# Kernel tuning notes

Measured on AMD Instinct MI355X. Metric: run time of the kernel, lower is better.

Reference implementation:

```python
import jax, jax.numpy as jnp
import numpy as np

NEG = -1000000.0


def setup_inputs() -> dict:
    key = jax.random.key(0)
    k0, k1, k2, k3, k4 = jax.random.split(key, 5)
    b, c, h, w = 4, 256, 64, 64
    dvt_c = 768
    x = jax.random.normal(k0, (b, c, h, w), jnp.float32)
    dvtfeats = jax.random.normal(k1, (b, dvt_c, h, w), jnp.float32)
    coarse = (jax.random.uniform(k2, (b, 1, h, w)) > 0.5).astype(jnp.float32)
    mask = jnp.repeat(jnp.repeat(coarse, 8, axis=2), 8, axis=3)  # [b,1,512,512]
    # K_conv: Conv2d(c+768 -> c, 1x1) with bias; fuse: Conv2d(2c -> c, 1x1) no bias
    K_w = jax.random.normal(k3, (c, c + dvt_c), jnp.float32) * 0.02
    K_b = jnp.zeros((c,), jnp.float32)
    fuse_w = jax.random.normal(k4, (c, 2 * c), jnp.float32) * 0.02
    return {"x": x, "mask": mask, "dvtfeats": dvtfeats, "K_w": K_w, "K_b": K_b, "fuse_w": fuse_w}


def _conv1x1(inp, w, b=None):
    out = jnp.einsum('bihw,oi->bohw', inp, w)
    if b is not None:
        out = out + b[None, :, None, None]
    return out


def _forward(x, mask, dvtfeats, K_w, K_b, fuse_w):
    b, c, h, w = x.shape
    n = h * w
    # maxpool(8,8) then binarize
    m = mask.reshape(b, 1, h, 8, w, 8).max(axis=(3, 5))
    m = (m > 0).astype(x.dtype)            # [b,1,h,w] foreground mask
    bm = 1.0 - m                            # background mask
    # K_conv applied once (original applies the same conv twice to the same input)
    feats = _conv1x1(jnp.concatenate([x, dvtfeats], axis=1), K_w, K_b)  # [b,c,h,w]
    K = (feats * bm).reshape(b, c, n)
    Q = (feats * m).reshape(b, c, n).transpose(0, 2, 1)  # [b,n,c]
    K = K / (jnp.linalg.norm(K, axis=1, keepdims=True) + 1e-8)
    Q = Q / (jnp.linalg.norm(Q, axis=2, keepdims=True) + 1e-8)
    V = (x * bm).reshape(b, c, n)
    score = jnp.einsum('bqc,bck->bqk', Q, K) * 20.0       # [b,n,n] cosine sims
    qm = m.reshape(b, 1, n)    # query mask (foreground)
    km = bm.reshape(b, 1, n)   # key mask (background)
    score = score + (1.0 - km) * NEG + (1.0 - qm).transpose(0, 2, 1) * NEG
    att = jax.nn.softmax(score, axis=-1)
    att = att * qm.transpose(0, 2, 1) * km                # zero out invalid rows/cols
    # att_fore[b,c,q] = sum_k V[b,c,k] * att[b,q,k]
    att_fore = jnp.einsum('bck,bqk->bcq', V, att).reshape(b, c, h, w)
    fused = _conv1x1(jnp.concatenate([att_fore, x], axis=1), fuse_w)
    visatt = att.sum(axis=1).reshape(b, 1, h, w)          # sum over query dim
    attmask = jnp.repeat(jnp.repeat(visatt, 8, axis=2), 8, axis=3)  # nearest upsample x8
    attmask = attmask / attmask.max()
    out = fused * m + x * (1.0 - m)
    return out, attmask


def reference(x, mask, dvtfeats, K_w, K_b, fuse_w):
    return _forward(x, mask, dvtfeats, K_w, K_b, fuse_w)
```

## Files before the change

### kernel.cpp

```cpp
#include <hip/hip_runtime.h>
#include <hip/hip_bf16.h>

typedef __attribute__((ext_vector_type(8))) short short8;
typedef __attribute__((ext_vector_type(4))) float f32x4;
typedef unsigned int uint;
typedef unsigned short ushort;

constexpr int BATCH = 4;
constexpr int CH    = 256;
constexpr int N     = 4096;
constexpr int DVC   = 768;
constexpr int CIN   = 1024;
constexpr int KC    = 512;
constexpr int PBS   = 5 * 1024 * 1024;
constexpr int QCH   = 32;
constexpr int SPLITK = 4;

constexpr size_t OFF_M    = 0;
constexpr size_t OFF_INV  = 64ull << 10;
constexpr size_t OFF_VIS  = 128ull << 10;
constexpr size_t OFF_MAXV = 192ull << 10;
constexpr size_t OFF_CNT  = 196ull << 10;
constexpr size_t OFF_FGI  = 256ull << 10;
constexpr size_t OFF_BGI  = 320ull << 10;
constexpr size_t OFF_P2S  = 384ull << 10;
constexpr size_t OFF_KMC  = 448ull << 10;
constexpr size_t OFF_PART = 1ull << 20;
constexpr size_t OFF_KWB  = 5ull << 20;
constexpr size_t OFF_FWB  = OFF_KWB + (512ull << 10);
constexpr size_t OFF_XT   = 6ull << 20;
constexpr size_t OFF_QC   = 38ull << 20;
constexpr size_t OFF_KCC  = 46ull << 20;
constexpr size_t OFF_XC   = 54ull << 20;
constexpr size_t OFF_AFT  = 62ull << 20;
constexpr size_t OFF_P    = 70ull << 20;
constexpr size_t OFF_AFP  = 110ull << 20;

__device__ __forceinline__ ushort f2bf(float f) {
    __hip_bfloat16 h = __float2bfloat16(f);
    return __builtin_bit_cast(ushort, h);
}
__device__ __forceinline__ float bf2f(ushort u) {
    uint v = (uint)u << 16;
    return __builtin_bit_cast(float, v);
}

typedef const __attribute__((address_space(1))) uint* gptr_t;
typedef __attribute__((address_space(3))) uint* lptr_t;
__device__ __forceinline__ void gload_lds16(const void* g, void* l) {
    __builtin_amdgcn_global_load_lds((gptr_t)g, (lptr_t)l, 16, 0, 0);
}

template<int WM, int WN>
__device__ __forceinline__ void gemm_core(
    const ushort* __restrict__ A0, int lda, int m0,
    const ushort* __restrict__ B0, int ldb0, int kend0,
    const ushort* __restrict__ B1, int ldb1,
    int n0, int K,
    ushort* AsL, ushort* BsL, f32x4 acc[4][4])
{
    constexpr int NW = WM * WN, BM = WM * 64, BN = WN * 64;
    const int t = threadIdx.x, lane = t & 63, wid = t >> 6;
    const int wm = (wid / WN) * 64, wn = (wid % WN) * 64;

    for (int k0 = 0; k0 < K; k0 += 64) {
        #pragma unroll
        for (int c = wid; c < BM / 8; c += NW) {
            const ushort* g = A0 + (size_t)(m0 + c * 8 + (lane >> 3)) * lda + (k0 + (lane & 7) * 8);
            gload_lds16(g, AsL + c * 512);
        }
        const ushort* Bsrc = (k0 < kend0) ? B0 : B1;
        const int ldb = (k0 < kend0) ? ldb0 : ldb1;
        const int kc  = (k0 < kend0) ? k0 : (k0 - kend0);
        #pragma unroll
        for (int c = wid; c < BN / 8; c += NW) {
            const ushort* g = Bsrc + (size_t)(n0 + c * 8 + (lane >> 3)) * ldb + (kc + (lane & 7) * 8);
            gload_lds16(g, BsL + c * 512);
        }
        __syncthreads();

        const int ra = wm + (lane & 15), rb = wn + (lane & 15), ko = (lane >> 4) * 8;
        #pragma unroll
        for (int kk = 0; kk < 64; kk += 32) {
            short8 a[4], b[4];
            #pragma unroll
            for (int i = 0; i < 4; i++) a[i] = *(const short8*)(AsL + (ra + i * 16) * 64 + kk + ko);
            #pragma unroll
            for (int j = 0; j < 4; j++) b[j] = *(const short8*)(BsL + (rb + j * 16) * 64 + kk + ko);
            #pragma unroll
            for (int i = 0; i < 4; i++)
                #pragma unroll
                for (int j = 0; j < 4; j++)
                    acc[i][j] = __builtin_amdgcn_mfma_f32_16x16x32_bf16(a[i], b[j], acc[i][j], 0, 0, 0);
        }
        __syncthreads();
    }
}

__device__ __forceinline__ void zero_acc(f32x4 acc[4][4]) {
    f32x4 z = {0.f, 0.f, 0.f, 0.f};
    #pragma unroll
    for (int i = 0; i < 4; i++)
        #pragma unroll
        for (int j = 0; j < 4; j++) acc[i][j] = z;
}

__global__ void k_maskpool(const float* __restrict__ mask, float* __restrict__ m,
                           float* __restrict__ vis, uint* __restrict__ maxv)
{
    int idx = blockIdx.x * 256 + threadIdx.x;
    int b = idx >> 12, p = idx & 4095;
    int y = p >> 6, x = p & 63;
    const float* base = mask + (size_t)b * 512 * 512 + (y * 8) * 512 + x * 8;
    float mx = 0.f;
    for (int dy = 0; dy < 8; dy++) {
        #pragma unroll
        for (int dx = 0; dx < 8; dx++) mx = fmaxf(mx, base[dy * 512 + dx]);
    }
    m[idx] = (mx > 0.f) ? 1.f : 0.f;
    vis[idx] = 0.f;
    if (idx == 0) maxv[0] = 0u;
}

__global__ __launch_bounds__(256) void k_scan(
    const float* __restrict__ m, int* __restrict__ fgi, int* __restrict__ bgi,
    int* __restrict__ counts, float* __restrict__ kmc, int* __restrict__ p2s)
{
    const int b = blockIdx.x, t = threadIdx.x;
    const float* mb = m + (size_t)b * N;
    __shared__ int sfg[256], sbg[256];
    bool isf[16];
    int cf = 0, cb_ = 0;
    #pragma unroll
    for (int j = 0; j < 16; j++) {
        bool f = mb[t * 16 + j] != 0.f;
        isf[j] = f; cf += f ? 1 : 0; cb_ += f ? 0 : 1;
    }
    sfg[t] = cf; sbg[t] = cb_;
    __syncthreads();
    for (int off = 1; off < 256; off <<= 1) {
        int vf = (t >= off) ? sfg[t - off] : 0;
        int vb = (t >= off) ? sbg[t - off] : 0;
        __syncthreads();
        sfg[t] += vf; sbg[t] += vb;
        __syncthreads();
    }
    int basef = sfg[t] - cf, baseb = sbg[t] - cb_;
    int nfg = sfg[255], nbg = sbg[255];
    #pragma unroll
    for (int j = 0; j < 16; j++) {
        int p = t * 16 + j;
        if (isf[j]) { fgi[b * N + basef] = p; p2s[b * N + p] = basef | (1 << 30); basef++; }
        else        { bgi[b * N + baseb] = p; p2s[b * N + p] = baseb; baseb++; }
    }
    if (t == 0) {
        counts[b * 4 + 0] = nfg;
        counts[b * 4 + 1] = (nfg + 127) & ~127;
        counts[b * 4 + 2] = nbg;
        counts[b * 4 + 3] = (nbg + 127) & ~127;
    }
    for (int j = t; j < N; j += 256) kmc[b * N + j] = (j < nbg) ? 1.f : 0.f;
}

__global__ void k_wconv(const float* __restrict__ Kw, const float* __restrict__ fw,
                        ushort* __restrict__ Kwb, ushort* __restrict__ fwb)
{
    int i = blockIdx.x * 256 + threadIdx.x;
    if (i < CH * CIN) Kwb[i] = f2bf(Kw[i]);
    else              fwb[i - CH * CIN] = f2bf(fw[i - CH * CIN]);
}

__global__ __launch_bounds__(256) void k_tr(const float* __restrict__ src,
                                            ushort* __restrict__ dst, int C)
{
    __shared__ float Ls[64][65];
    const int ci0 = blockIdx.x * 64, n0 = blockIdx.y * 64, b = blockIdx.z;
    const float* s = src + (size_t)b * C * 4096;
    const int t = threadIdx.x;
    #pragma unroll
    for (int it = 0; it < 4; it++) {
        int f4 = it * 256 + t;
        int r = f4 >> 4, c4 = f4 & 15;
        float4 v = *(const float4*)(s + (size_t)(ci0 + r) * 4096 + n0 + c4 * 4);
        Ls[r][c4 * 4 + 0] = v.x; Ls[r][c4 * 4 + 1] = v.y;
        Ls[r][c4 * 4 + 2] = v.z; Ls[r][c4 * 4 + 3] = v.w;
    }
    __syncthreads();
    ushort* d = dst + (size_t)b * 4096 * C;
    #pragma unroll
    for (int it = 0; it < 8; it++) {
        int p = it * 256 + t;
        int rn = p >> 5, cc2 = p & 31;
        uint val = (uint)f2bf(Ls[cc2 * 2][rn]) | ((uint)f2bf(Ls[cc2 * 2 + 1][rn]) << 16);
        *(uint*)(d + (size_t)(n0 + rn) * C + ci0 + cc2 * 2) = val;
    }
}

__global__ __launch_bounds__(256) void k_vgather(
    const ushort* __restrict__ xT, const int* __restrict__ bgi,
    const int* __restrict__ counts, ushort* __restrict__ xc)
{
    __shared__ ushort Xs[64][264];
    const int b = blockIdx.y;
    const int ki0 = blockIdx.x * 64;
    const int nbg = counts[b * 4 + 2], nbgp = counts[b * 4 + 3];
    if (ki0 >= nbgp) return;
    const int t = threadIdx.x;
    const int j = t >> 2, part = t & 3;
    const int ki = ki0 + j;
    if (ki < nbg) {
        const ushort* src = xT + ((size_t)b * N + bgi[(size_t)b * N + ki]) * CH + part * 64;
        #pragma unroll
        for (int q = 0; q < 8; q++)
            *(uint4*)&Xs[j][part * 64 + q * 8] = *(const uint4*)(src + q * 8);
    } else {
        uint4 z = {0, 0, 0, 0};
        #pragma unroll
        for (int q = 0; q < 8; q++)
            *(uint4*)&Xs[j][part * 64 + q * 8] = z;
    }
    __syncthreads();
    const int c = t;
    ushort* dst = xc + ((size_t)b * CH + c) * N + ki0;
    uint w[32];
    #pragma unroll
    for (int jj = 0; jj < 32; jj++)
        w[jj] = (uint)Xs[2 * jj][c] | ((uint)Xs[2 * jj + 1][c] << 16);
    #pragma unroll
    for (int q = 0; q < 8; q++) {
        uint4 o = { w[q * 4], w[q * 4 + 1], w[q * 4 + 2], w[q * 4 + 3] };
        *(uint4*)(dst + q * 8) = o;
    }
}

__global__ __launch_bounds__(256) void k_feats(
    const ushort* __restrict__ Kwb, const ushort* __restrict__ xT,
    const float* __restrict__ dvt, const float* __restrict__ Kb,
    const int* __restrict__ p2s, ushort* __restrict__ Qc, ushort* __restrict__ Kc)
{
    __shared__ ushort As[256 * 64];
    __shared__ ushort Bs[64 * 64];
    __shared__ float  Ls[64][65];
    __shared__ float  red[4][64];
    const int b = blockIdx.z;
    const int n0 = blockIdx.x * 64;
    const int t = threadIdx.x, lane = t & 63, wid = t >> 6;
    const ushort* xTb = xT + (size_t)b * N * CH;
    const float* dvb = dvt + (size_t)b * DVC * N;
    f32x4 acc[4][4]; zero_acc(acc);

    for (int k0 = 0; k0 < 256; k0 += 64) {
        #pragma unroll
        for (int c = wid; c < 32; c += 4)
            gload_lds16(Kwb + (size_t)(c * 8 + (lane >> 3)) * CIN + k0 + (lane & 7) * 8, As + c * 512);
        #pragma unroll
        for (int c = wid; c < 8; c += 4)
            gload_lds16(xTb + (size_t)(n0 + c * 8 + (lane >> 3)) * CH + k0 + (lane & 7) * 8, Bs + c * 512);
        __syncthreads();
        const int ra = wid * 64 + (lane & 15), rb = lane & 15, ko = (lane >> 4) * 8;
        #pragma unroll
        for (int kk = 0; kk < 64; kk += 32) {
            short8 a[4], bb[4];
            #pragma unroll
            for (int i = 0; i < 4; i++) a[i] = *(const short8*)(As + (ra + i * 16) * 64 + kk + ko);
            #pragma unroll
            for (int j = 0; j < 4; j++) bb[j] = *(const short8*)(Bs + (rb + j * 16) * 64 + kk + ko);
            #pragma unroll
            for (int i = 0; i < 4; i++)
                #pragma unroll
                for (int j = 0; j < 4; j++)
                    acc[i][j] = __builtin_amdgcn_mfma_f32_16x16x32_bf16(a[i], bb[j], acc[i][j], 0, 0, 0);
        }
        __syncthreads();
    }
    for (int k0 = 256; k0 < 1024; k0 += 64) {
        #pragma unroll
        for (int c = wid; c < 32; c += 4)
            gload_lds16(Kwb + (size_t)(c * 8 + (lane >> 3)) * CIN + k0 + (lane & 7) * 8, As + c * 512);
        const float* dsrc = dvb + (size_t)(k0 - 256) * N + n0;
        #pragma unroll
        for (int it = 0; it < 4; it++) {
            int f4 = it * 256 + t;
            int r = f4 >> 4, c4 = (f4 & 15) * 4;
            float4 v = *(const float4*)(dsrc + (size_t)r * N + c4);
            Ls[r][c4 + 0] = v.x; Ls[r][c4 + 1] = v.y;
            Ls[r][c4 + 2] = v.z; Ls[r][c4 + 3] = v.w;
        }
        __syncthreads();
        {
            int rn = t >> 2;
            int ks = (t & 3) * 16;
            #pragma unroll
            for (int j2 = 0; j2 < 8; j2++) {
                int kk = ks + j2 * 2;
                uint val = (uint)f2bf(Ls[kk][rn]) | ((uint)f2bf(Ls[kk + 1][rn]) << 16);
                int idx = (rn * 64 + kk) ^ ((rn & 7) << 3);
                *(uint*)(Bs + idx) = val;
            }
        }
        __syncthreads();
        const int ra = wid * 64 + (lane & 15), rb = lane & 15, ko = (lane >> 4) * 8;
        #pragma unroll
        for (int kk = 0; kk < 64; kk += 32) {
            short8 a[4], bb[4];
            #pragma unroll
            for (int i = 0; i < 4; i++) a[i] = *(const short8*)(As + (ra + i * 16) * 64 + kk + ko);
            #pragma unroll
            for (int j = 0; j < 4; j++) {
                int row = rb + j * 16;
                int idx = (row * 64 + kk + ko) ^ ((row & 7) << 3);
                bb[j] = *(const short8*)(Bs + idx);
            }
            #pragma unroll
            for (int i = 0; i < 4; i++)
                #pragma unroll
                for (int j = 0; j < 4; j++)
                    acc[i][j] = __builtin_amdgcn_mfma_f32_16x16x32_bf16(a[i], bb[j], acc[i][j], 0, 0, 0);
        }
        __syncthreads();
    }

    const int wm = wid * 64;
    float sj[4] = {0.f, 0.f, 0.f, 0.f};
    #pragma unroll
    for (int i = 0; i < 4; i++) {
        int mbase = wm + i * 16 + ((lane >> 4) * 4);
        float4 bias = *(const float4*)(Kb + mbase);
        #pragma unroll
        for (int j = 0; j < 4; j++) {
            acc[i][j][0] += bias.x; acc[i][j][1] += bias.y;
            acc[i][j][2] += bias.z; acc[i][j][3] += bias.w;
            sj[j] += acc[i][j][0] * acc[i][j][0] + acc[i][j][1] * acc[i][j][1]
                   + acc[i][j][2] * acc[i][j][2] + acc[i][j][3] * acc[i][j][3];
        }
    }
    #pragma unroll
    for (int j = 0; j < 4; j++) {
        sj[j] += __shfl_xor(sj[j], 16);
        sj[j] += __shfl_xor(sj[j], 32);
    }
    if (lane < 16) {
        #pragma unroll
        for (int j = 0; j < 4; j++) red[wid][j * 16 + lane] = sj[j];
    }
    __syncthreads();
    const int* pb = p2s + (size_t)b * N + n0;
    #pragma unroll
    for (int j = 0; j < 4; j++) {
        int n = j * 16 + (lane & 15);
        float s = red[0][n] + red[1][n] + red[2][n] + red[3][n];
        float invn = 1.f / (sqrtf(s) + 1e-8f);
        int sl = pb[n];
        ushort* dst = (sl & (1 << 30)) ? Qc : Kc;
        int slot = sl & 0x3FFFFFFF;
        ushort* drow = dst + ((size_t)b * N + slot) * CH;
        #pragma unroll
        for (int i = 0; i < 4; i++) {
            int mbase = wm + i * 16 + ((lane >> 4) * 4);
            ushort4 o = { f2bf(acc[i][j][0] * invn), f2bf(acc[i][j][1] * invn),
                          f2bf(acc[i][j][2] * invn), f2bf(acc[i][j][3] * invn) };
            *(ushort4*)(drow + mbase) = o;
        }
    }
}

__global__ __launch_bounds__(128) void k_score(
    const ushort* __restrict__ Qc, const ushort* __restrict__ Kc,
    const float* __restrict__ kmc, const int* __restrict__ counts,
    ushort* __restrict__ P)
{
    const int b = blockIdx.z;
    const int nfgp = counts[b * 4 + 1], nbgp = counts[b * 4 + 3];
    const int m0 = blockIdx.y * 128;
    const int n0 = blockIdx.x * 64;
    if (m0 >= nfgp || n0 >= nbgp) return;
    __shared__ ushort SH[(128 + 64) * 64];
    const int t = threadIdx.x, lane = t & 63, wid = t >> 6;
    const ushort* Qb = Qc + (size_t)b * N * CH;
    const ushort* Kb_ = Kc + (size_t)b * N * CH;
    f32x4 acc[4][4]; zero_acc(acc);
    gemm_core<2, 1>(Qb, CH, m0, Kb_, CH, CH, Kb_, CH, n0, CH, SH, SH + 128 * 64, acc);

    const int wm = wid * 64;
    float km[4];
    #pragma unroll
    for (int j = 0; j < 4; j++) km[j] = kmc[(size_t)b * N + n0 + j * 16 + (lane & 15)];

    ushort* Cs = SH;
    #pragma unroll
    for (int i = 0; i < 4; i++) {
        int rbase = wm + i * 16 + ((lane >> 4) * 4);
        #pragma unroll
        for (int j = 0; j < 4; j++) {
            int cl = j * 16 + (lane & 15);
            #pragma unroll
            for (int r = 0; r < 4; r++) {
                float p = (km[j] != 0.f) ? __expf(20.f * acc[i][j][r] - 20.f) : 0.f;
                Cs[(rbase + r) * 64 + cl] = f2bf(p);
            }
        }
    }
    __syncthreads();
    ushort* Pb = P + (size_t)b * PBS;
    #pragma unroll
    for (int it = 0; it < 8; it++) {
        int v8 = it * 128 + t;
        int row = v8 >> 3, c8 = (v8 & 7) * 8;
        *(uint4*)(Pb + (size_t)(m0 + row) * nbgp + n0 + c8) = *(const uint4*)(Cs + row * 64 + c8);
    }
}

__global__ __launch_bounds__(256) void k_rowsum(
    const ushort* __restrict__ P, const int* __restrict__ counts,
    float* __restrict__ inv)
{
    const int t = threadIdx.x, lane = t & 63, wid = t >> 6;
    const int g = blockIdx.x * 4 + wid;
    const int b = g >> 12, qi = g & 4095;
    const int nfgp = counts[b * 4 + 1], nbgp = counts[b * 4 + 3];
    if (qi >= nfgp) return;
    const ushort* row = P + (size_t)b * PBS + (size_t)qi * nbgp;
    float s = 0.f;
    for (int it = 0; it < 8; it++) {
        int base = it * 512 + lane * 8;
        if (base < nbgp) {
            uint4 v = *(const uint4*)(row + base);
            const ushort* u = (const ushort*)&v;
            #pragma unroll
            for (int e = 0; e < 8; e++) s += bf2f(u[e]);
        }
    }
    #pragma unroll
    for (int mm = 1; mm < 64; mm <<= 1) s += __shfl_xor(s, mm);
    if (lane == 0) inv[g] = (s > 0.f) ? 1.f / s : 0.f;
}

__global__ __launch_bounds__(256) void k_att_fore(
    const ushort* __restrict__ xc, const ushort* __restrict__ P,
    const int* __restrict__ counts, ushort* __restrict__ AFp)
{
    const int b = blockIdx.z & (BATCH - 1);
    const int sk = blockIdx.z / BATCH;
    const int nfgp = counts[b * 4 + 1], nbgp = counts[b * 4 + 3];
    const int n0 = blockIdx.x * 64;
    if (n0 >= nfgp) return;
    const int kchunk = ((nbgp / 64 + SPLITK - 1) / SPLITK) * 64;
    const int k0s = sk * kchunk;
    const int len = min(kchunk, nbgp - k0s);

    const int lane = threadIdx.x & 63, wid = threadIdx.x >> 6;
    f32x4 acc[4][4]; zero_acc(acc);
    if (len > 0) {
        __shared__ ushort SH[(256 + 64) * 64];
        const ushort* Pb = P + (size_t)b * PBS + k0s;
        gemm_core<4, 1>(xc + (size_t)b * CH * N + k0s, N, 0,
                        Pb, nbgp, 1 << 30, Pb, nbgp,
                        n0, len, SH, SH + 256 * 64, acc);
    }
    ushort* Ap = AFp + ((size_t)(sk * BATCH + b) * N) * CH;
    const int wm = wid * 64;
    #pragma unroll
    for (int j = 0; j < 4; j++) {
        int qi = n0 + j * 16 + (lane & 15);
        #pragma unroll
        for (int i = 0; i < 4; i++) {
            int mbase = wm + i * 16 + ((lane >> 4) * 4);
            ushort4 o = { f2bf(acc[i][j][0]), f2bf(acc[i][j][1]),
                          f2bf(acc[i][j][2]), f2bf(acc[i][j][3]) };
            *(ushort4*)(Ap + (size_t)qi * CH + mbase) = o;
        }
    }
}

__global__ __launch_bounds__(256) void k_afreduce(
    const ushort* __restrict__ AFp, const float* __restrict__ inv,
    const int* __restrict__ fgi, const int* __restrict__ counts,
    ushort* __restrict__ AFt)
{
    const int t = threadIdx.x, lane = t & 63, wid = t >> 6;
    const int g = blockIdx.x * 4 + wid;
    const int b = g >> 12, qi = g & 4095;
    if (qi >= counts[b * 4]) return;
    const size_t rowoff = ((size_t)b * N + qi) * CH + lane * 4;
    float s0 = 0.f, s1 = 0.f, s2 = 0.f, s3 = 0.f;
    #pragma unroll
    for (int sk = 0; sk < SPLITK; sk++) {
        ushort4 v = *(const ushort4*)(AFp + (size_t)sk * BATCH * N * CH + rowoff);
        s0 += bf2f(v.x); s1 += bf2f(v.y); s2 += bf2f(v.z); s3 += bf2f(v.w);
    }
    float iq = inv[g];
    int q = fgi[g];
    ushort4 o = { f2bf(s0 * iq), f2bf(s1 * iq), f2bf(s2 * iq), f2bf(s3 * iq) };
    *(ushort4*)(AFt + ((size_t)b * N + q) * CH + lane * 4) = o;
}

__global__ __launch_bounds__(128) void k_fused(
    const ushort* __restrict__ fwb, const ushort* __restrict__ AFt,
    const ushort* __restrict__ xT, const float* __restrict__ x,
    const float* __restrict__ m_, float* __restrict__ out)
{
    __shared__ ushort SH[(64 + 128) * 64];
    const int b = blockIdx.z;
    const int n0 = blockIdx.x * 128, m0 = blockIdx.y * 64;
    const int lane = threadIdx.x & 63, wid = threadIdx.x >> 6;
    const int wn = (wid & 1) * 64;
    f32x4 acc[4][4]; zero_acc(acc);
    gemm_core<1, 2>(fwb, KC, m0,
                    AFt + (size_t)b * N * CH, CH, CH,
                    xT + (size_t)b * N * CH, CH,
                    n0, KC, SH, SH + 64 * 64, acc);
    const float* mb = m_ + (size_t)b * N;
    const float* xc_ = x + (size_t)b * CH * N;
    float* ob = out + (size_t)b * CH * N;
    #pragma unroll
    for (int j = 0; j < 4; j++) {
        int n = n0 + wn + j * 16 + (lane & 15);
        float mv = mb[n];
        #pragma unroll
        for (int i = 0; i < 4; i++) {
            int mbase = m0 + i * 16 + ((lane >> 4) * 4);
            #pragma unroll
            for (int r = 0; r < 4; r++) {
                int c = mbase + r;
                ob[(size_t)c * N + n] = (mv != 0.f) ? acc[i][j][r] : xc_[(size_t)c * N + n];
            }
        }
    }
}

__global__ __launch_bounds__(256) void k_colsum(
    const ushort* __restrict__ P, const float* __restrict__ inv,
    const int* __restrict__ counts, float* __restrict__ part)
{
    const int b = blockIdx.z, qc = blockIdx.y, t = threadIdx.x;
    const int nfg = counts[b * 4], nbgp = counts[b * 4 + 3];
    const int ki0 = blockIdx.x * 2048 + t * 8;
    if (ki0 >= nbgp) return;
    const int qchunk = (nfg + QCH - 1) / QCH;
    const int q0 = qc * qchunk, q1 = min(q0 + qchunk, nfg);
    const ushort* base = P + (size_t)b * PBS + (size_t)q0 * nbgp + ki0;
    const float* ib = inv + (size_t)b * N;
    float acc[8] = {};
    int q = q0;
    for (; q + 4 <= q1; q += 4) {
        uint4 v0 = *(const uint4*)(base);
        uint4 v1 = *(const uint4*)(base + (size_t)nbgp);
        uint4 v2 = *(const uint4*)(base + 2 * (size_t)nbgp);
        uint4 v3 = *(const uint4*)(base + 3 * (size_t)nbgp);
        float i0 = ib[q], i1 = ib[q + 1], i2 = ib[q + 2], i3 = ib[q + 3];
        const ushort* u0 = (const ushort*)&v0;
        const ushort* u1 = (const ushort*)&v1;
        const ushort* u2 = (const ushort*)&v2;
        const ushort* u3 = (const ushort*)&v3;
        #pragma unroll
        for (int e = 0; e < 8; e++)
            acc[e] += bf2f(u0[e]) * i0 + bf2f(u1[e]) * i1 + bf2f(u2[e]) * i2 + bf2f(u3[e]) * i3;
        base += 4 * (size_t)nbgp;
    }
    for (; q < q1; q++) {
        uint4 v = *(const uint4*)(base);
        float iq = ib[q];
        const ushort* u = (const ushort*)&v;
        #pragma unroll
        for (int e = 0; e < 8; e++) acc[e] += bf2f(u[e]) * iq;
        base += (size_t)nbgp;
    }
    float* pp = part + (size_t)qc * (BATCH * N) + (size_t)b * N + ki0;
    float4 o0 = {acc[0], acc[1], acc[2], acc[3]};
    float4 o1 = {acc[4], acc[5], acc[6], acc[7]};
    *(float4*)(pp)     = o0;
    *(float4*)(pp + 4) = o1;
}

__global__ void k_colsum_final(const float* __restrict__ part, const int* __restrict__ bgi,
                               const int* __restrict__ counts, float* __restrict__ vis,
                               uint* __restrict__ maxv)
{
    int g = blockIdx.x * 256 + threadIdx.x;
    int b = g >> 12, ki = g & 4095;
    int t = threadIdx.x;
    float s = 0.f;
    if (ki < counts[b * 4 + 2]) {
        #pragma unroll
        for (int j = 0; j < QCH; j++) s += part[(size_t)j * (BATCH * N) + g];
        vis[(size_t)b * N + bgi[(size_t)b * N + ki]] = s;
    }
    __shared__ float red[256];
    red[t] = s; __syncthreads();
    for (int st = 128; st > 0; st >>= 1) { if (t < st) red[t] = fmaxf(red[t], red[t + st]); __syncthreads(); }
    if (t == 0) atomicMax(maxv, __float_as_uint(red[0]));
}

__global__ void k_attmask(const float* __restrict__ vis, const float* __restrict__ maxv,
                          float* __restrict__ amask)
{
    int idx = blockIdx.x * 256 + threadIdx.x;
    int b = idx >> 18;
    int r = idx & 262143;
    int Y = r >> 9, X = r & 511;
    amask[idx] = vis[(size_t)b * N + (Y >> 3) * 64 + (X >> 3)] / maxv[0];
}

extern "C" void kernel_launch(void* const* d_in, const int* in_sizes, int n_in,
                              void* d_out, int out_size, void* d_ws, size_t ws_size,
                              hipStream_t stream)
{
    const float* x    = (const float*)d_in[0];
    const float* mask = (const float*)d_in[1];
    const float* dvt  = (const float*)d_in[2];
    const float* Kw   = (const float*)d_in[3];
    const float* Kb   = (const float*)d_in[4];
    const float* fw   = (const float*)d_in[5];
    float* out = (float*)d_out;

    char* ws = (char*)d_ws;
    float*  m    = (float*)(ws + OFF_M);
    float*  inv  = (float*)(ws + OFF_INV);
    float*  vis  = (float*)(ws + OFF_VIS);
    float*  maxv = (float*)(ws + OFF_MAXV);
    int*    cnt  = (int*)  (ws + OFF_CNT);
    int*    fgi  = (int*)  (ws + OFF_FGI);
    int*    bgi  = (int*)  (ws + OFF_BGI);
    int*    p2s  = (int*)  (ws + OFF_P2S);
    float*  kmc  = (float*)(ws + OFF_KMC);
    float*  part = (float*)(ws + OFF_PART);
    ushort* Kwb  = (ushort*)(ws + OFF_KWB);
    ushort* fwb  = (ushort*)(ws + OFF_FWB);
    ushort* xT   = (ushort*)(ws + OFF_XT);
    ushort* Qc   = (ushort*)(ws + OFF_QC);
    ushort* Kcc  = (ushort*)(ws + OFF_KCC);
    ushort* xc   = (ushort*)(ws + OFF_XC);
    ushort* AFt  = (ushort*)(ws + OFF_AFT);
    ushort* P    = (ushort*)(ws + OFF_P);
    ushort* AFp  = (ushort*)(ws + OFF_AFP);

    k_maskpool   <<<dim3(BATCH * N / 256), 256, 0, stream>>>(mask, m, vis, (uint*)maxv);
    k_scan       <<<dim3(BATCH), 256, 0, stream>>>(m, fgi, bgi, cnt, kmc, p2s);
    k_wconv      <<<dim3((CH * CIN + CH * KC) / 256), 256, 0, stream>>>(Kw, fw, Kwb, fwb);
    k_tr         <<<dim3(CH / 64, 64, BATCH), 256, 0, stream>>>(x, xT, CH);
    k_feats      <<<dim3(N / 64, 1, BATCH), 256, 0, stream>>>(Kwb, xT, dvt, Kb, p2s, Qc, Kcc);
    k_vgather    <<<dim3(N / 64, BATCH), 256, 0, stream>>>(xT, bgi, cnt, xc);
    k_score      <<<dim3(N / 64, N / 128, BATCH), 128, 0, stream>>>(Qc, Kcc, kmc, cnt, P);
    k_rowsum     <<<dim3(BATCH * N / 4), 256, 0, stream>>>(P, cnt, inv);
    k_att_fore   <<<dim3(N / 64, 1, BATCH * SPLITK), 256, 0, stream>>>(xc, P, cnt, AFp);
    k_afreduce   <<<dim3(BATCH * N / 4), 256, 0, stream>>>(AFp, inv, fgi, cnt, AFt);
    k_colsum     <<<dim3(2, QCH, BATCH), 256, 0, stream>>>(P, inv, cnt, part);
    k_colsum_final<<<dim3(BATCH * N / 256), 256, 0, stream>>>(part, bgi, cnt, vis, (uint*)maxv);
    k_fused      <<<dim3(N / 128, CH / 64, BATCH), 128, 0, stream>>>(fwb, AFt, xT, x, m, out);
    k_attmask    <<<dim3(BATCH * 512 * 512 / 256), 256, 0, stream>>>(vis, maxv, out + (size_t)BATCH * CH * N);
}
```

Before: 170.2 us.

## Fuse row sums into score kernel, split feats GEMM, merge prep kernels

Row sums of the exponentiated scores are computed inside the score kernel and written as per-tile partials, so a tiny kernel reduces them and the full re-read of P is avoided. The feature GEMM is split across two M halves for more blocks, with normalization and scatter moved into a separate pass over a bf16 intermediate. Mask pooling and weight conversion share one launch. The split adds an extra 8MB round trip and normalizes from bf16-rounded values.

```diff
diff --git a/kernel.cpp b/kernel.cpp
--- a/kernel.cpp
+++ b/kernel.cpp
@@ -35,6 +35,7 @@
 constexpr size_t OFF_AFT  = 62ull << 20;
 constexpr size_t OFF_P    = 70ull << 20;
 constexpr size_t OFF_AFP  = 110ull << 20;
+constexpr size_t OFF_FT   = 142ull << 20;
 
 __device__ __forceinline__ ushort f2bf(float f) {
     __hip_bfloat16 h = __float2bfloat16(f);
@@ -105,21 +106,30 @@
         for (int j = 0; j < 4; j++) acc[i][j] = z;
 }
 
-__global__ void k_maskpool(const float* __restrict__ mask, float* __restrict__ m,
-                           float* __restrict__ vis, uint* __restrict__ maxv)
-{
-    int idx = blockIdx.x * 256 + threadIdx.x;
-    int b = idx >> 12, p = idx & 4095;
-    int y = p >> 6, x = p & 63;
-    const float* base = mask + (size_t)b * 512 * 512 + (y * 8) * 512 + x * 8;
-    float mx = 0.f;
-    for (int dy = 0; dy < 8; dy++) {
-        #pragma unroll
-        for (int dx = 0; dx < 8; dx++) mx = fmaxf(mx, base[dy * 512 + dx]);
-    }
-    m[idx] = (mx > 0.f) ? 1.f : 0.f;
-    vis[idx] = 0.f;
-    if (idx == 0) maxv[0] = 0u;
+__global__ void k_prep(const float* __restrict__ mask, const float* __restrict__ Kw,
+                       const float* __restrict__ fw, float* __restrict__ m,
+                       float* __restrict__ vis, uint* __restrict__ maxv,
+                       ushort* __restrict__ Kwb, ushort* __restrict__ fwb)
+{
+    const int bid = blockIdx.x;
+    if (bid < 64) {
+        int idx = bid * 256 + threadIdx.x;
+        int b = idx >> 12, p = idx & 4095;
+        int y = p >> 6, x = p & 63;
+        const float* base = mask + (size_t)b * 512 * 512 + (y * 8) * 512 + x * 8;
+        float mx = 0.f;
+        for (int dy = 0; dy < 8; dy++) {
+            #pragma unroll
+            for (int dx = 0; dx < 8; dx++) mx = fmaxf(mx, base[dy * 512 + dx]);
+        }
+        m[idx] = (mx > 0.f) ? 1.f : 0.f;
+        vis[idx] = 0.f;
+        if (idx == 0) maxv[0] = 0u;
+    } else {
+        int i = (bid - 64) * 256 + threadIdx.x;
+        if (i < CH * CIN) Kwb[i] = f2bf(Kw[i]);
+        else              fwb[i - CH * CIN] = f2bf(fw[i - CH * CIN]);
+    }
 }
 
 __global__ __launch_bounds__(256) void k_scan(
@@ -160,14 +170,6 @@
         counts[b * 4 + 3] = (nbg + 127) & ~127;
     }
     for (int j = t; j < N; j += 256) kmc[b * N + j] = (j < nbg) ? 1.f : 0.f;
-}
-
-__global__ void k_wconv(const float* __restrict__ Kw, const float* __restrict__ fw,
-                        ushort* __restrict__ Kwb, ushort* __restrict__ fwb)
-{
-    int i = blockIdx.x * 256 + threadIdx.x;
-    if (i < CH * CIN) Kwb[i] = f2bf(Kw[i]);
-    else              fwb[i - CH * CIN] = f2bf(fw[i - CH * CIN]);
 }
 
 __global__ __launch_bounds__(256) void k_tr(const float* __restrict__ src,
@@ -233,16 +235,16 @@
     }
 }
 
-__global__ __launch_bounds__(256) void k_feats(
+__global__ __launch_bounds__(128) void k_featsA(
     const ushort* __restrict__ Kwb, const ushort* __restrict__ xT,
     const float* __restrict__ dvt, const float* __restrict__ Kb,
-    const int* __restrict__ p2s, ushort* __restrict__ Qc, ushort* __restrict__ Kc)
-{
-    __shared__ ushort As[256 * 64];
+    ushort* __restrict__ Ft)
+{
+    __shared__ ushort As[128 * 64];
     __shared__ ushort Bs[64 * 64];
     __shared__ float  Ls[64][65];
-    __shared__ float  red[4][64];
     const int b = blockIdx.z;
+    const int m0 = blockIdx.y * 128;
     const int n0 = blockIdx.x * 64;
     const int t = threadIdx.x, lane = t & 63, wid = t >> 6;
     const ushort* xTb = xT + (size_t)b * N * CH;
@@ -251,10 +253,10 @@
 
     for (int k0 = 0; k0 < 256; k0 += 64) {
         #pragma unroll
-        for (int c = wid; c < 32; c += 4)
-            gload_lds16(Kwb + (size_t)(c * 8 + (lane >> 3)) * CIN + k0 + (lane & 7) * 8, As + c * 512);
-        #pragma unroll
-        for (int c = wid; c < 8; c += 4)
+        for (int c = wid; c < 16; c += 2)
+            gload_lds16(Kwb + (size_t)(m0 + c * 8 + (lane >> 3)) * CIN + k0 + (lane & 7) * 8, As + c * 512);
+        #pragma unroll
+        for (int c = wid; c < 8; c += 2)
             gload_lds16(xTb + (size_t)(n0 + c * 8 + (lane >> 3)) * CH + k0 + (lane & 7) * 8, Bs + c * 512);
         __syncthreads();
         const int ra = wid * 64 + (lane & 15), rb = lane & 15, ko = (lane >> 4) * 8;
@@ -275,12 +277,12 @@
     }
     for (int k0 = 256; k0 < 1024; k0 += 64) {
         #pragma unroll
-        for (int c = wid; c < 32; c += 4)
-            gload_lds16(Kwb + (size_t)(c * 8 + (lane >> 3)) * CIN + k0 + (lane & 7) * 8, As + c * 512);
+        for (int c = wid; c < 16; c += 2)
+            gload_lds16(Kwb + (size_t)(m0 + c * 8 + (lane >> 3)) * CIN + k0 + (lane & 7) * 8, As + c * 512);
         const float* dsrc = dvb + (size_t)(k0 - 256) * N + n0;
         #pragma unroll
-        for (int it = 0; it < 4; it++) {
-            int f4 = it * 256 + t;
+        for (int it = 0; it < 8; it++) {
+            int f4 = it * 128 + t;
             int r = f4 >> 4, c4 = (f4 & 15) * 4;
             float4 v = *(const float4*)(dsrc + (size_t)r * N + c4);
             Ls[r][c4 + 0] = v.x; Ls[r][c4 + 1] = v.y;
@@ -288,10 +290,10 @@
         }
         __syncthreads();
         {
-            int rn = t >> 2;
-            int ks = (t & 3) * 16;
-            #pragma unroll
-            for (int j2 = 0; j2 < 8; j2++) {
+            int rn = t >> 1;
+            int ks = (t & 1) * 32;
+            #pragma unroll
+            for (int j2 = 0; j2 < 16; j2++) {
                 int kk = ks + j2 * 2;
                 uint val = (uint)f2bf(Ls[kk][rn]) | ((uint)f2bf(Ls[kk + 1][rn]) << 16);
                 int idx = (rn * 64 + kk) ^ ((rn & 7) << 3);
@@ -320,54 +322,46 @@
         __syncthreads();
     }
 
-    const int wm = wid * 64;
-    float sj[4] = {0.f, 0.f, 0.f, 0.f};
+    const int wm = m0 + wid * 64;
+    ushort* Fb = Ft + (size_t)b * N * CH;
     #pragma unroll
     for (int i = 0; i < 4; i++) {
         int mbase = wm + i * 16 + ((lane >> 4) * 4);
         float4 bias = *(const float4*)(Kb + mbase);
         #pragma unroll
         for (int j = 0; j < 4; j++) {
-            acc[i][j][0] += bias.x; acc[i][j][1] += bias.y;
-            acc[i][j][2] += bias.z; acc[i][j][3] += bias.w;
-            sj[j] += acc[i][j][0] * acc[i][j][0] + acc[i][j][1] * acc[i][j][1]
-                   + acc[i][j][2] * acc[i][j][2] + acc[i][j][3] * acc[i][j][3];
-        }
-    }
-    #pragma unroll
-    for (int j = 0; j < 4; j++) {
-        sj[j] += __shfl_xor(sj[j], 16);
-        sj[j] += __shfl_xor(sj[j], 32);
-    }
-    if (lane < 16) {
-        #pragma unroll
-        for (int j = 0; j < 4; j++) red[wid][j * 16 + lane] = sj[j];
-    }
-    __syncthreads();
-    const int* pb = p2s + (size_t)b * N + n0;
-    #pragma unroll
-    for (int j = 0; j < 4; j++) {
-        int n = j * 16 + (lane & 15);
-        float s = red[0][n] + red[1][n] + red[2][n] + red[3][n];
-        float invn = 1.f / (sqrtf(s) + 1e-8f);
-        int sl = pb[n];
-        ushort* dst = (sl & (1 << 30)) ? Qc : Kc;
-        int slot = sl & 0x3FFFFFFF;
-        ushort* drow = dst + ((size_t)b * N + slot) * CH;
-        #pragma unroll
-        for (int i = 0; i < 4; i++) {
-            int mbase = wm + i * 16 + ((lane >> 4) * 4);
-            ushort4 o = { f2bf(acc[i][j][0] * invn), f2bf(acc[i][j][1] * invn),
-                          f2bf(acc[i][j][2] * invn), f2bf(acc[i][j][3] * invn) };
-            *(ushort4*)(drow + mbase) = o;
-        }
-    }
+            int n = n0 + j * 16 + (lane & 15);
+            ushort4 o = { f2bf(acc[i][j][0] + bias.x), f2bf(acc[i][j][1] + bias.y),
+                          f2bf(acc[i][j][2] + bias.z), f2bf(acc[i][j][3] + bias.w) };
+            *(ushort4*)(Fb + (size_t)n * CH + mbase) = o;
+        }
+    }
+}
+
+__global__ __launch_bounds__(256) void k_norm2(
+    const ushort* __restrict__ Ft, const int* __restrict__ p2s,
+    ushort* __restrict__ Qc, ushort* __restrict__ Kc)
+{
+    const int t = threadIdx.x, lane = t & 63, wid = t >> 6;
+    const int g = blockIdx.x * 4 + wid;
+    const int b = g >> 12;
+    ushort4 v = *(const ushort4*)(Ft + (size_t)g * CH + lane * 4);
+    float f0 = bf2f(v.x), f1 = bf2f(v.y), f2 = bf2f(v.z), f3 = bf2f(v.w);
+    float s = f0 * f0 + f1 * f1 + f2 * f2 + f3 * f3;
+    #pragma unroll
+    for (int mm = 1; mm < 64; mm <<= 1) s += __shfl_xor(s, mm);
+    float invn = 1.f / (sqrtf(s) + 1e-8f);
+    int sl = p2s[g];
+    ushort* dst = (sl & (1 << 30)) ? Qc : Kc;
+    int slot = sl & 0x3FFFFFFF;
+    ushort4 o = { f2bf(f0 * invn), f2bf(f1 * invn), f2bf(f2 * invn), f2bf(f3 * invn) };
+    *(ushort4*)(dst + ((size_t)b * N + slot) * CH + lane * 4) = o;
 }
 
 __global__ __launch_bounds__(128) void k_score(
     const ushort* __restrict__ Qc, const ushort* __restrict__ Kc,
     const float* __restrict__ kmc, const int* __restrict__ counts,
-    ushort* __restrict__ P)
+    ushort* __restrict__ P, float* __restrict__ rowpart)
 {
     const int b = blockIdx.z;
     const int nfgp = counts[b * 4 + 1], nbgp = counts[b * 4 + 3];
@@ -387,6 +381,7 @@
     for (int j = 0; j < 4; j++) km[j] = kmc[(size_t)b * N + n0 + j * 16 + (lane & 15)];
 
     ushort* Cs = SH;
+    float sir[4][4] = {};
     #pragma unroll
     for (int i = 0; i < 4; i++) {
         int rbase = wm + i * 16 + ((lane >> 4) * 4);
@@ -397,8 +392,26 @@
             for (int r = 0; r < 4; r++) {
                 float p = (km[j] != 0.f) ? __expf(20.f * acc[i][j][r] - 20.f) : 0.f;
                 Cs[(rbase + r) * 64 + cl] = f2bf(p);
+                sir[i][r] += p;
             }
         }
+    }
+    #pragma unroll
+    for (int i = 0; i < 4; i++)
+        #pragma unroll
+        for (int r = 0; r < 4; r++) {
+            float s = sir[i][r];
+            s += __shfl_xor(s, 1); s += __shfl_xor(s, 2);
+            s += __shfl_xor(s, 4); s += __shfl_xor(s, 8);
+            sir[i][r] = s;
+        }
+    if ((lane & 15) == 0) {
+        float* rp = rowpart + (size_t)(n0 >> 6) * (BATCH * N) + (size_t)b * N + m0;
+        #pragma unroll
+        for (int i = 0; i < 4; i++)
+            #pragma unroll
+            for (int r = 0; r < 4; r++)
+                rp[wm + i * 16 + ((lane >> 4) * 4) + r] = sir[i][r];
     }
     __syncthreads();
     ushort* Pb = P + (size_t)b * PBS;
@@ -410,29 +423,17 @@
     }
 }
 
-__global__ __launch_bounds__(256) void k_rowsum(
-    const ushort* __restrict__ P, const int* __restrict__ counts,
-    float* __restrict__ inv)
-{
-    const int t = threadIdx.x, lane = t & 63, wid = t >> 6;
-    const int g = blockIdx.x * 4 + wid;
-    const int b = g >> 12, qi = g & 4095;
-    const int nfgp = counts[b * 4 + 1], nbgp = counts[b * 4 + 3];
+__global__ void k_rowinv(const float* __restrict__ rowpart, const int* __restrict__ counts,
+                         float* __restrict__ inv)
+{
+    int g = blockIdx.x * 256 + threadIdx.x;
+    int b = g >> 12, qi = g & 4095;
+    int nfgp = counts[b * 4 + 1], nbgp = counts[b * 4 + 3];
     if (qi >= nfgp) return;
-    const ushort* row = P + (size_t)b * PBS + (size_t)qi * nbgp;
+    int nsl = nbgp >> 6;
     float s = 0.f;
-    for (int it = 0; it < 8; it++) {
-        int base = it * 512 + lane * 8;
-        if (base < nbgp) {
-            uint4 v = *(const uint4*)(row + base);
-            const ushort* u = (const ushort*)&v;
-            #pragma unroll
-            for (int e = 0; e < 8; e++) s += bf2f(u[e]);
-        }
-    }
-    #pragma unroll
-    for (int mm = 1; mm < 64; mm <<= 1) s += __shfl_xor(s, mm);
-    if (lane == 0) inv[g] = (s > 0.f) ? 1.f / s : 0.f;
+    for (int sl = 0; sl < nsl; sl++) s += rowpart[(size_t)sl * (BATCH * N) + g];
+    inv[g] = (s > 0.f) ? 1.f / s : 0.f;
 }
 
 __global__ __launch_bounds__(256) void k_att_fore(
@@ -633,15 +634,17 @@
     ushort* AFt  = (ushort*)(ws + OFF_AFT);
     ushort* P    = (ushort*)(ws + OFF_P);
     ushort* AFp  = (ushort*)(ws + OFF_AFP);
-
-    k_maskpool   <<<dim3(BATCH * N / 256), 256, 0, stream>>>(mask, m, vis, (uint*)maxv);
+    ushort* Ft   = (ushort*)(ws + OFF_FT);
+
+    k_prep       <<<dim3(64 + (CH * CIN + CH * KC) / 256), 256, 0, stream>>>(
+                     mask, Kw, fw, m, vis, (uint*)maxv, Kwb, fwb);
     k_scan       <<<dim3(BATCH), 256, 0, stream>>>(m, fgi, bgi, cnt, kmc, p2s);
-    k_wconv      <<<dim3((CH * CIN + CH * KC) / 256), 256, 0, stream>>>(Kw, fw, Kwb, fwb);
     k_tr         <<<dim3(CH / 64, 64, BATCH), 256, 0, stream>>>(x, xT, CH);
-    k_feats      <<<dim3(N / 64, 1, BATCH), 256, 0, stream>>>(Kwb, xT, dvt, Kb, p2s, Qc, Kcc);
+    k_featsA     <<<dim3(N / 64, 2, BATCH), 128, 0, stream>>>(Kwb, xT, dvt, Kb, Ft);
+    k_norm2      <<<dim3(BATCH * N / 4), 256, 0, stream>>>(Ft, p2s, Qc, Kcc);
     k_vgather    <<<dim3(N / 64, BATCH), 256, 0, stream>>>(xT, bgi, cnt, xc);
-    k_score      <<<dim3(N / 64, N / 128, BATCH), 128, 0, stream>>>(Qc, Kcc, kmc, cnt, P);
-    k_rowsum     <<<dim3(BATCH * N / 4), 256, 0, stream>>>(P, cnt, inv);
+    k_score      <<<dim3(N / 64, N / 128, BATCH), 128, 0, stream>>>(Qc, Kcc, kmc, cnt, P, part);
+    k_rowinv     <<<dim3(BATCH * N / 256), 256, 0, stream>>>(part, cnt, inv);
     k_att_fore   <<<dim3(N / 64, 1, BATCH * SPLITK), 256, 0, stream>>>(xc, P, cnt, AFp);
     k_afreduce   <<<dim3(BATCH * N / 4), 256, 0, stream>>>(AFp, inv, fgi, cnt, AFt);
     k_colsum     <<<dim3(2, QCH, BATCH), 256, 0, stream>>>(P, inv, cnt, part);
```

After: 177.3 us. 1.04x slower.
